# Performance work log

Measured on AMD Instinct MI355X. Metric: run time of the kernel, lower is better.

The kernel has to match this reference:

```python
import jax, jax.numpy as jnp
import numpy as np

# Sampled-neighborhood cascade sizes (src->dst per layer) and edge counts
N0, N1, N2, N3 = 400000, 200000, 100000, 50000
E1, E2, E3 = 500000, 300000, 150000
DIN, DH = 128, 128


def setup_inputs() -> dict:
    key = jax.random.key(0)
    ks = jax.random.split(key, 24)
    inp = {}
    inp['x'] = jax.random.normal(ks[0], (N0, DIN), jnp.float32)
    inp['src1'] = jax.random.randint(ks[1], (E1,), 0, N0, dtype=jnp.int64)
    inp['dst1'] = jax.random.randint(ks[2], (E1,), 0, N1, dtype=jnp.int64)
    inp['src2'] = jax.random.randint(ks[3], (E2,), 0, N1, dtype=jnp.int64)
    inp['dst2'] = jax.random.randint(ks[4], (E2,), 0, N2, dtype=jnp.int64)
    inp['src3'] = jax.random.randint(ks[5], (E3,), 0, N2, dtype=jnp.int64)
    inp['dst3'] = jax.random.randint(ks[6], (E3,), 0, N3, dtype=jnp.int64)
    # SAGEConv params: lin_l (on aggregated neighbors, with bias), lin_r (root, no bias)
    dims = [(DIN, DH), (DH, DH), (DH, DH)]
    for i, (di, do) in enumerate(dims, start=1):
        s = 1.0 / np.sqrt(di)
        inp[f'Wl{i}'] = jax.random.uniform(ks[6 + 4 * i - 3], (di, do), jnp.float32, -s, s)
        inp[f'Wr{i}'] = jax.random.uniform(ks[6 + 4 * i - 2], (di, do), jnp.float32, -s, s)
        inp[f'b{i}'] = jax.random.uniform(ks[6 + 4 * i - 1], (do,), jnp.float32, -s, s)
        inp[f'a{i}'] = jnp.full((do,), 0.25, jnp.float32)  # PReLU per-channel init
    return inp


def _sage_prelu(x_src, n_dst, src, dst, Wl, Wr, b, alpha):
    # mean aggregation over incoming edges (PyG SAGEConv default aggr='mean')
    x_dst = x_src[:n_dst]                                   # [n_dst, d]
    msg = x_src[src]                                        # [E, d] gather
    summed = jax.ops.segment_sum(msg, dst, num_segments=n_dst)
    cnt = jax.ops.segment_sum(jnp.ones(src.shape[0], x_src.dtype), dst,
                              num_segments=n_dst)
    mean = summed / jnp.maximum(cnt, 1.0)[:, None]
    out = mean @ Wl + b + x_dst @ Wr                        # lin_l(aggr) + lin_r(root)
    return jnp.where(out > 0, out, alpha * out)             # per-channel PReLU


def reference(x, src1, dst1, src2, dst2, src3, dst3,
              Wl1, Wr1, b1, a1, Wl2, Wr2, b2, a2, Wl3, Wr3, b3, a3):
    h = _sage_prelu(x, N1, src1, dst1, Wl1, Wr1, b1, a1)
    h = _sage_prelu(h, N2, src2, dst2, Wl2, Wr2, b2, a2)
    h = _sage_prelu(h, N3, src3, dst3, Wl3, Wr3, b3, a3)
    return h  # [N3, DH]
```

## Files before the change

### kernel.cpp

```cpp
#include <hip/hip_runtime.h>


constexpr int cN0 = 400000, cN1 = 200000, cN2 = 100000, cN3 = 50000;
constexpr int cE1 = 500000, cE2 = 300000, cE3 = 150000;
constexpr int cNT = cN1 + cN2 + cN3;
constexpr int cET = cE1 + cE2 + cE3;

#define NDIV_UP(a, b) (((a) + (b) - 1) / (b))

typedef __attribute__((ext_vector_type(8))) short bf16x8;
typedef __attribute__((ext_vector_type(4))) float f32x4;
typedef __attribute__((ext_vector_type(4))) unsigned u32x4;

__device__ __forceinline__ unsigned fbits(float f) {
  return __builtin_bit_cast(unsigned, f);
}
__device__ __forceinline__ float ffrom(unsigned u) {
  return __builtin_bit_cast(float, u);
}
__device__ __forceinline__ unsigned short f2bf(float f) {
  unsigned u = fbits(f);
  unsigned r = u + 0x7FFFu + ((u >> 16) & 1u);
  return (unsigned short)(r >> 16);
}
__device__ __forceinline__ float bf2f(unsigned short h) {
  return ffrom((unsigned)h << 16);
}

__global__ void detect_idx64_kernel(const long long* __restrict__ p, int E,
                                    long long nmax, int* __restrict__ flag) {
  int t = threadIdx.x;
  int n = E < 512 ? E : 512;
  int bad = 0;
  for (int i = t; i < n; i += 64) {
    long long v = p[i];
    if (v < 0 || v >= nmax) bad = 1;
  }
  unsigned long long b = __ballot(bad);
  if (t == 0) *flag = (b == 0ull) ? 1 : 0;
}

__device__ __forceinline__ int load_idx(const void* p, int i, int flag) {
  return flag ? (int)((const long long*)p)[i] : ((const int*)p)[i];
}

__global__ void hist3_kernel(const void* __restrict__ d1, const void* __restrict__ d2,
                             const void* __restrict__ d3, const int* __restrict__ flag,
                             int* __restrict__ CNT) {
  int e = blockIdx.x * 256 + threadIdx.x;
  if (e >= cET) return;
  int f = *flag;
  int d;
  if (e < cE1) d = load_idx(d1, e, f);
  else if (e < cE1 + cE2) d = cN1 + load_idx(d2, e - cE1, f);
  else d = cN1 + cN2 + load_idx(d3, e - cE1 - cE2, f);
  atomicAdd(&CNT[d], 1);
}

__global__ __launch_bounds__(256) void scan_reduce(const int* __restrict__ cnt,
                                                   int n, int* __restrict__ bsum) {
  __shared__ int s[256];
  int t = threadIdx.x;
  int base = blockIdx.x * 1024 + t * 4;
  int v = 0;
  if (base + 3 < n) {
    int4 c = *(const int4*)(cnt + base);
    v = c.x + c.y + c.z + c.w;
  } else {
    for (int i = 0; i < 4; ++i)
      if (base + i < n) v += cnt[base + i];
  }
  s[t] = v;
  __syncthreads();
  for (int off = 128; off > 0; off >>= 1) {
    if (t < off) s[t] += s[t + off];
    __syncthreads();
  }
  if (t == 0) bsum[blockIdx.x] = s[0];
}

__global__ __launch_bounds__(256) void scan_bsums(int* __restrict__ bsum, int nb) {
  __shared__ int s[256];
  int t = threadIdx.x;
  int v0 = (2 * t < nb) ? bsum[2 * t] : 0;
  int v1 = (2 * t + 1 < nb) ? bsum[2 * t + 1] : 0;
  int p = v0 + v1;
  s[t] = p;
  __syncthreads();
  for (int off = 1; off < 256; off <<= 1) {
    int x = (t >= off) ? s[t - off] : 0;
    __syncthreads();
    s[t] += x;
    __syncthreads();
  }
  int excl = s[t] - p;
  if (2 * t < nb) bsum[2 * t] = excl;
  if (2 * t + 1 < nb) bsum[2 * t + 1] = excl + v0;
}

__global__ __launch_bounds__(256) void scan_final(const int* __restrict__ cnt,
                                                  int n, const int* __restrict__ bsum,
                                                  int* __restrict__ offs) {
  __shared__ int s[256];
  int t = threadIdx.x;
  int base = blockIdx.x * 1024 + t * 4;
  int v0 = 0, v1 = 0, v2 = 0, v3 = 0;
  if (base + 3 < n) {
    int4 c = *(const int4*)(cnt + base);
    v0 = c.x; v1 = c.y; v2 = c.z; v3 = c.w;
  } else {
    if (base + 0 < n) v0 = cnt[base + 0];
    if (base + 1 < n) v1 = cnt[base + 1];
    if (base + 2 < n) v2 = cnt[base + 2];
  }
  int tsum = v0 + v1 + v2 + v3;
  s[t] = tsum;
  __syncthreads();
  for (int off = 1; off < 256; off <<= 1) {
    int x = (t >= off) ? s[t - off] : 0;
    __syncthreads();
    s[t] += x;
    __syncthreads();
  }
  int excl = s[t] - tsum;
  int o = bsum[blockIdx.x] + excl;
  if (base + 0 < n) offs[base + 0] = o;
  o += v0;
  if (base + 1 < n) offs[base + 1] = o;
  o += v1;
  if (base + 2 < n) offs[base + 2] = o;
  o += v2;
  if (base + 3 < n) offs[base + 3] = o;
}

__global__ void fill3_kernel(const void* __restrict__ s1, const void* __restrict__ d1,
                             const void* __restrict__ s2, const void* __restrict__ d2,
                             const void* __restrict__ s3, const void* __restrict__ d3,
                             const int* __restrict__ flag,
                             int* __restrict__ OFFS, int* __restrict__ EID) {
  int e = blockIdx.x * 256 + threadIdx.x;
  if (e >= cET) return;
  int f = *flag;
  int s, d;
  if (e < cE1) {
    s = load_idx(s1, e, f);
    d = load_idx(d1, e, f);
  } else if (e < cE1 + cE2) {
    int i = e - cE1;
    s = load_idx(s2, i, f);
    d = cN1 + load_idx(d2, i, f);
  } else {
    int i = e - cE1 - cE2;
    s = load_idx(s3, i, f);
    d = cN1 + cN2 + load_idx(d3, i, f);
  }
  int pos = atomicAdd(&OFFS[d], 1);
  EID[pos] = s;
}

__global__ void pack_w3_kernel(const float* __restrict__ Wl1, const float* __restrict__ Wr1,
                               const float* __restrict__ Wl2, const float* __restrict__ Wr2,
                               const float* __restrict__ Wl3, const float* __restrict__ Wr3,
                               unsigned short* __restrict__ wpk) {
  int idx = blockIdx.x * 256 + threadIdx.x;
  if (idx >= 3 * 16384) return;
  int L = idx >> 14;
  int r = idx & 16383;
  const float* Wl = L == 0 ? Wl1 : (L == 1 ? Wl2 : Wl3);
  const float* Wr = L == 0 ? Wr1 : (L == 1 ? Wr2 : Wr3);
  unsigned short* o = wpk + L * 32768;
  int j = r & 7, l = (r >> 3) & 63, cf = (r >> 9) & 7, ks = r >> 12;
  int k = ks * 32 + (l >> 4) * 8 + j;
  int col = cf * 16 + (l & 15);
  o[r] = f2bf(Wl[k * 128 + col]);
  o[16384 + r] = f2bf(Wr[k * 128 + col]);
}

__global__ __launch_bounds__(256) void fused_kernel(
    const float* __restrict__ hsrc, const int* __restrict__ OFFS,
    const int* __restrict__ EID, int rowoff,
    const unsigned short* __restrict__ W,
    const float* __restrict__ bias, const float* __restrict__ alpha,
    float* __restrict__ out, int n) {
  const int lane = threadIdx.x & 63;
  const int wv = threadIdx.x >> 6;
  const int rbase = blockIdx.x * 128 + wv * 32;
  const int g = lane >> 4;
  const int r16 = lane & 15;

  bf16x8 mh[2][4], ml[2][4];
#pragma unroll
  for (int t = 0; t < 2; ++t) {
    const int row = rbase + t * 16 + r16;
    float s[4][8];
#pragma unroll
    for (int ks = 0; ks < 4; ++ks)
#pragma unroll
      for (int j = 0; j < 8; ++j) s[ks][j] = 0.f;
    int start = 0, end = 0;
    if (row < n) {
      int gr = rowoff + row;
      start = gr ? OFFS[gr - 1] : 0;
      end = OFFS[gr];
    }
    for (int i = start; i < end; ++i) {
      const float* rp = hsrc + (size_t)EID[i] * 128 + g * 8;
#pragma unroll
      for (int ks = 0; ks < 4; ++ks) {
        const float4 v0 = *(const float4*)(rp + ks * 32);
        const float4 v1 = *(const float4*)(rp + ks * 32 + 4);
        s[ks][0] += v0.x; s[ks][1] += v0.y; s[ks][2] += v0.z; s[ks][3] += v0.w;
        s[ks][4] += v1.x; s[ks][5] += v1.y; s[ks][6] += v1.z; s[ks][7] += v1.w;
      }
    }
    const float inv = (end > start) ? 1.0f / (float)(end - start) : 0.0f;
#pragma unroll
    for (int ks = 0; ks < 4; ++ks) {
      u32x4 hwv, lwv;
#pragma unroll
      for (int p = 0; p < 4; ++p) {
        float me = s[ks][2 * p] * inv, mo = s[ks][2 * p + 1] * inv;
        unsigned ue = fbits(me), uo = fbits(mo);
        hwv[p] = (ue >> 16) | (uo & 0xFFFF0000u);
        float re = me - ffrom(ue & 0xFFFF0000u);
        float ro = mo - ffrom(uo & 0xFFFF0000u);
        lwv[p] = (fbits(re) >> 16) | (fbits(ro) & 0xFFFF0000u);
      }
      mh[t][ks] = __builtin_bit_cast(bf16x8, hwv);
      ml[t][ks] = __builtin_bit_cast(bf16x8, lwv);
    }
  }

  f32x4 acc[2][8] = {};
  for (int ks = 0; ks < 4; ++ks) {
    bf16x8 xh[2], xl[2];
#pragma unroll
    for (int t = 0; t < 2; ++t) {
      const int row = rbase + t * 16 + r16;
      if (row < n) {
        const float* xp = hsrc + (size_t)row * 128 + ks * 32 + g * 8;
        float xv[8];
        *(float4*)&xv[0] = *(const float4*)(xp);
        *(float4*)&xv[4] = *(const float4*)(xp + 4);
        u32x4 hwv, lwv;
#pragma unroll
        for (int p = 0; p < 4; ++p) {
          unsigned ue = fbits(xv[2 * p]), uo = fbits(xv[2 * p + 1]);
          hwv[p] = (ue >> 16) | (uo & 0xFFFF0000u);
          float re = xv[2 * p] - ffrom(ue & 0xFFFF0000u);
          float ro = xv[2 * p + 1] - ffrom(uo & 0xFFFF0000u);
          lwv[p] = (fbits(re) >> 16) | (fbits(ro) & 0xFFFF0000u);
        }
        xh[t] = __builtin_bit_cast(bf16x8, hwv);
        xl[t] = __builtin_bit_cast(bf16x8, lwv);
      } else {
        xh[t] = (bf16x8)0;
        xl[t] = (bf16x8)0;
      }
    }
    const unsigned short* wb = W + (size_t)ks * 4096 + (size_t)lane * 8;
#pragma unroll
    for (int cf = 0; cf < 8; ++cf) {
      const unsigned short* wp = wb + cf * 512;
      bf16x8 wl = *(const bf16x8*)(wp);
      bf16x8 wr = *(const bf16x8*)(wp + 16384);
#pragma unroll
      for (int t = 0; t < 2; ++t) {
        acc[t][cf] = __builtin_amdgcn_mfma_f32_16x16x32_bf16(mh[t][ks], wl, acc[t][cf], 0, 0, 0);
        acc[t][cf] = __builtin_amdgcn_mfma_f32_16x16x32_bf16(ml[t][ks], wl, acc[t][cf], 0, 0, 0);
        acc[t][cf] = __builtin_amdgcn_mfma_f32_16x16x32_bf16(xh[t], wr, acc[t][cf], 0, 0, 0);
        acc[t][cf] = __builtin_amdgcn_mfma_f32_16x16x32_bf16(xl[t], wr, acc[t][cf], 0, 0, 0);
      }
    }
  }

  const int ocol0 = lane & 15;
  const int orow_off = (lane >> 4) * 4;
#pragma unroll
  for (int cf = 0; cf < 8; ++cf) {
    const int ocol = cf * 16 + ocol0;
    const float b = bias[ocol];
    const float a = alpha[ocol];
#pragma unroll
    for (int t = 0; t < 2; ++t) {
      const int orb = rbase + t * 16 + orow_off;
#pragma unroll
      for (int i = 0; i < 4; ++i) {
        const int orow = orb + i;
        if (orow < n) {
          float v = acc[t][cf][i] + b;
          out[(size_t)orow * 128 + ocol] = v > 0.f ? v : a * v;
        }
      }
    }
  }
}

extern "C" void kernel_launch(void* const* d_in, const int* in_sizes, int n_in,
                              void* d_out, int out_size, void* d_ws, size_t ws_size,
                              hipStream_t stream) {
  const float* x = (const float*)d_in[0];
  const void* src1 = d_in[1];
  const void* dst1 = d_in[2];
  const void* src2 = d_in[3];
  const void* dst2 = d_in[4];
  const void* src3 = d_in[5];
  const void* dst3 = d_in[6];
  const float* Wl1 = (const float*)d_in[7];
  const float* Wr1 = (const float*)d_in[8];
  const float* b1  = (const float*)d_in[9];
  const float* a1  = (const float*)d_in[10];
  const float* Wl2 = (const float*)d_in[11];
  const float* Wr2 = (const float*)d_in[12];
  const float* b2  = (const float*)d_in[13];
  const float* a2  = (const float*)d_in[14];
  const float* Wl3 = (const float*)d_in[15];
  const float* Wr3 = (const float*)d_in[16];
  const float* b3  = (const float*)d_in[17];
  const float* a3  = (const float*)d_in[18];

  float* R1 = (float*)d_ws;
  float* R2 = R1 + (size_t)cN1 * 128;
  int* CNT = (int*)(R2 + (size_t)cN2 * 128);
  int* OFFS = CNT + cNT;
  int* EID = OFFS + cNT;
  int* bsum = EID + cET;
  int* flag = bsum + 1024;
  unsigned short* wpk = (unsigned short*)(flag + 64);

  const int nb = NDIV_UP(cNT, 1024);

  detect_idx64_kernel<<<1, 64, 0, stream>>>((const long long*)src1, cE1,
                                            (long long)cN0, flag);
  pack_w3_kernel<<<192, 256, 0, stream>>>(Wl1, Wr1, Wl2, Wr2, Wl3, Wr3, wpk);
  hipMemsetAsync(CNT, 0, (size_t)cNT * sizeof(int), stream);
  hist3_kernel<<<NDIV_UP(cET, 256), 256, 0, stream>>>(dst1, dst2, dst3, flag, CNT);
  scan_reduce<<<nb, 256, 0, stream>>>(CNT, cNT, bsum);
  scan_bsums<<<1, 256, 0, stream>>>(bsum, nb);
  scan_final<<<nb, 256, 0, stream>>>(CNT, cNT, bsum, OFFS);
  fill3_kernel<<<NDIV_UP(cET, 256), 256, 0, stream>>>(src1, dst1, src2, dst2,
                                                      src3, dst3, flag, OFFS, EID);

  fused_kernel<<<NDIV_UP(cN1, 128), 256, 0, stream>>>(
      x, OFFS, EID, 0, wpk, b1, a1, R1, cN1);
  fused_kernel<<<NDIV_UP(cN2, 128), 256, 0, stream>>>(
      R1, OFFS, EID, cN1, wpk + 32768, b2, a2, R2, cN2);
  fused_kernel<<<NDIV_UP(cN3, 128), 256, 0, stream>>>(
      R2, OFFS, EID, cN1 + cN2, wpk + 65536, b3, a3, (float*)d_out, cN3);
}
```

Before: 410.1 us.

## Split gather from GEMM, store bf16 intermediates, drop hi/lo split MFMA

```diff
diff --git a/kernel.cpp b/kernel.cpp
--- a/kernel.cpp
+++ b/kernel.cpp
@@ -22,9 +22,6 @@
   unsigned u = fbits(f);
   unsigned r = u + 0x7FFFu + ((u >> 16) & 1u);
   return (unsigned short)(r >> 16);
-}
-__device__ __forceinline__ float bf2f(unsigned short h) {
-  return ffrom((unsigned)h << 16);
 }
 
 __global__ void detect_idx64_kernel(const long long* __restrict__ p, int E,
@@ -176,86 +173,87 @@
   o[16384 + r] = f2bf(Wr[k * 128 + col]);
 }
 
-__global__ __launch_bounds__(256) void fused_kernel(
-    const float* __restrict__ hsrc, const int* __restrict__ OFFS,
+template <bool SRCF32>
+__global__ __launch_bounds__(256) void gather_kernel(
+    const void* __restrict__ hsrc, const int* __restrict__ OFFS,
     const int* __restrict__ EID, int rowoff,
+    unsigned short* __restrict__ meanB, int n) {
+  int row = blockIdx.x * 4 + (threadIdx.x >> 6);
+  if (row >= n) return;
+  int lane = threadIdx.x & 63;
+  int gr = rowoff + row;
+  int start = gr ? OFFS[gr - 1] : 0;
+  int end = OFFS[gr];
+  float a0 = 0.f, a1 = 0.f, b0 = 0.f, b1 = 0.f;
+  int i = start;
+  for (; i + 1 < end; i += 2) {
+    int s0 = EID[i], s1 = EID[i + 1];
+    if (SRCF32) {
+      float2 v0 = *(const float2*)((const float*)hsrc + (size_t)s0 * 128 + lane * 2);
+      float2 v1 = *(const float2*)((const float*)hsrc + (size_t)s1 * 128 + lane * 2);
+      a0 += v0.x; a1 += v0.y;
+      b0 += v1.x; b1 += v1.y;
+    } else {
+      unsigned u0 = *(const unsigned*)((const unsigned short*)hsrc + (size_t)s0 * 128 + lane * 2);
+      unsigned u1 = *(const unsigned*)((const unsigned short*)hsrc + (size_t)s1 * 128 + lane * 2);
+      a0 += ffrom(u0 << 16); a1 += ffrom(u0 & 0xFFFF0000u);
+      b0 += ffrom(u1 << 16); b1 += ffrom(u1 & 0xFFFF0000u);
+    }
+  }
+  if (i < end) {
+    int s0 = EID[i];
+    if (SRCF32) {
+      float2 v0 = *(const float2*)((const float*)hsrc + (size_t)s0 * 128 + lane * 2);
+      a0 += v0.x; a1 += v0.y;
+    } else {
+      unsigned u0 = *(const unsigned*)((const unsigned short*)hsrc + (size_t)s0 * 128 + lane * 2);
+      a0 += ffrom(u0 << 16); a1 += ffrom(u0 & 0xFFFF0000u);
+    }
+  }
+  a0 += b0; a1 += b1;
+  float inv = (end > start) ? 1.0f / (float)(end - start) : 0.0f;
+  unsigned o = (unsigned)f2bf(a0 * inv) | ((unsigned)f2bf(a1 * inv) << 16);
+  *(unsigned*)(meanB + (size_t)row * 128 + lane * 2) = o;
+}
+
+template <bool XF32, bool OUTF32>
+__global__ __launch_bounds__(256) void gemm_kernel(
+    const unsigned short* __restrict__ meanB, const void* __restrict__ xsrc,
     const unsigned short* __restrict__ W,
     const float* __restrict__ bias, const float* __restrict__ alpha,
-    float* __restrict__ out, int n) {
+    void* __restrict__ outp, int n) {
   const int lane = threadIdx.x & 63;
   const int wv = threadIdx.x >> 6;
   const int rbase = blockIdx.x * 128 + wv * 32;
   const int g = lane >> 4;
   const int r16 = lane & 15;
 
-  bf16x8 mh[2][4], ml[2][4];
-#pragma unroll
-  for (int t = 0; t < 2; ++t) {
-    const int row = rbase + t * 16 + r16;
-    float s[4][8];
-#pragma unroll
-    for (int ks = 0; ks < 4; ++ks)
-#pragma unroll
-      for (int j = 0; j < 8; ++j) s[ks][j] = 0.f;
-    int start = 0, end = 0;
-    if (row < n) {
-      int gr = rowoff + row;
-      start = gr ? OFFS[gr - 1] : 0;
-      end = OFFS[gr];
-    }
-    for (int i = start; i < end; ++i) {
-      const float* rp = hsrc + (size_t)EID[i] * 128 + g * 8;
-#pragma unroll
-      for (int ks = 0; ks < 4; ++ks) {
-        const float4 v0 = *(const float4*)(rp + ks * 32);
-        const float4 v1 = *(const float4*)(rp + ks * 32 + 4);
-        s[ks][0] += v0.x; s[ks][1] += v0.y; s[ks][2] += v0.z; s[ks][3] += v0.w;
-        s[ks][4] += v1.x; s[ks][5] += v1.y; s[ks][6] += v1.z; s[ks][7] += v1.w;
-      }
-    }
-    const float inv = (end > start) ? 1.0f / (float)(end - start) : 0.0f;
-#pragma unroll
-    for (int ks = 0; ks < 4; ++ks) {
-      u32x4 hwv, lwv;
-#pragma unroll
-      for (int p = 0; p < 4; ++p) {
-        float me = s[ks][2 * p] * inv, mo = s[ks][2 * p + 1] * inv;
-        unsigned ue = fbits(me), uo = fbits(mo);
-        hwv[p] = (ue >> 16) | (uo & 0xFFFF0000u);
-        float re = me - ffrom(ue & 0xFFFF0000u);
-        float ro = mo - ffrom(uo & 0xFFFF0000u);
-        lwv[p] = (fbits(re) >> 16) | (fbits(ro) & 0xFFFF0000u);
-      }
-      mh[t][ks] = __builtin_bit_cast(bf16x8, hwv);
-      ml[t][ks] = __builtin_bit_cast(bf16x8, lwv);
-    }
-  }
-
   f32x4 acc[2][8] = {};
+
   for (int ks = 0; ks < 4; ++ks) {
-    bf16x8 xh[2], xl[2];
+    bf16x8 am[2], ax[2];
 #pragma unroll
     for (int t = 0; t < 2; ++t) {
       const int row = rbase + t * 16 + r16;
       if (row < n) {
-        const float* xp = hsrc + (size_t)row * 128 + ks * 32 + g * 8;
-        float xv[8];
-        *(float4*)&xv[0] = *(const float4*)(xp);
-        *(float4*)&xv[4] = *(const float4*)(xp + 4);
-        u32x4 hwv, lwv;
-#pragma unroll
-        for (int p = 0; p < 4; ++p) {
-          unsigned ue = fbits(xv[2 * p]), uo = fbits(xv[2 * p + 1]);
-          hwv[p] = (ue >> 16) | (uo & 0xFFFF0000u);
-          float re = xv[2 * p] - ffrom(ue & 0xFFFF0000u);
-          float ro = xv[2 * p + 1] - ffrom(uo & 0xFFFF0000u);
-          lwv[p] = (fbits(re) >> 16) | (fbits(ro) & 0xFFFF0000u);
+        am[t] = *(const bf16x8*)(meanB + (size_t)row * 128 + ks * 32 + g * 8);
+        if (XF32) {
+          const float* xp = (const float*)xsrc + (size_t)row * 128 + ks * 32 + g * 8;
+          float xv[8];
+          *(float4*)&xv[0] = *(const float4*)(xp);
+          *(float4*)&xv[4] = *(const float4*)(xp + 4);
+          u32x4 w;
+#pragma unroll
+          for (int p = 0; p < 4; ++p) {
+            w[p] = (unsigned)f2bf(xv[2 * p]) | ((unsigned)f2bf(xv[2 * p + 1]) << 16);
+          }
+          ax[t] = __builtin_bit_cast(bf16x8, w);
+        } else {
+          ax[t] = *(const bf16x8*)((const unsigned short*)xsrc + (size_t)row * 128 + ks * 32 + g * 8);
         }
-        xh[t] = __builtin_bit_cast(bf16x8, hwv);
-        xl[t] = __builtin_bit_cast(bf16x8, lwv);
       } else {
-        xh[t] = (bf16x8)0;
-        xl[t] = (bf16x8)0;
+        am[t] = (bf16x8)0;
+        ax[t] = (bf16x8)0;
       }
     }
     const unsigned short* wb = W + (size_t)ks * 4096 + (size_t)lane * 8;
@@ -266,10 +264,8 @@
       bf16x8 wr = *(const bf16x8*)(wp + 16384);
 #pragma unroll
       for (int t = 0; t < 2; ++t) {
-        acc[t][cf] = __builtin_amdgcn_mfma_f32_16x16x32_bf16(mh[t][ks], wl, acc[t][cf], 0, 0, 0);
-        acc[t][cf] = __builtin_amdgcn_mfma_f32_16x16x32_bf16(ml[t][ks], wl, acc[t][cf], 0, 0, 0);
-        acc[t][cf] = __builtin_amdgcn_mfma_f32_16x16x32_bf16(xh[t], wr, acc[t][cf], 0, 0, 0);
-        acc[t][cf] = __builtin_amdgcn_mfma_f32_16x16x32_bf16(xl[t], wr, acc[t][cf], 0, 0, 0);
+        acc[t][cf] = __builtin_amdgcn_mfma_f32_16x16x32_bf16(am[t], wl, acc[t][cf], 0, 0, 0);
+        acc[t][cf] = __builtin_amdgcn_mfma_f32_16x16x32_bf16(ax[t], wr, acc[t][cf], 0, 0, 0);
       }
     }
   }
@@ -289,7 +285,12 @@
         const int orow = orb + i;
         if (orow < n) {
           float v = acc[t][cf][i] + b;
-          out[(size_t)orow * 128 + ocol] = v > 0.f ? v : a * v;
+          v = v > 0.f ? v : a * v;
+          if (OUTF32) {
+            ((float*)outp)[(size_t)orow * 128 + ocol] = v;
+          } else {
+            ((unsigned short*)outp)[(size_t)orow * 128 + ocol] = f2bf(v);
+          }
         }
       }
     }
@@ -319,9 +320,10 @@
   const float* b3  = (const float*)d_in[17];
   const float* a3  = (const float*)d_in[18];
 
-  float* R1 = (float*)d_ws;
-  float* R2 = R1 + (size_t)cN1 * 128;
-  int* CNT = (int*)(R2 + (size_t)cN2 * 128);
+  unsigned short* M1 = (unsigned short*)d_ws;
+  unsigned short* M2 = M1 + (size_t)cN1 * 128;
+  unsigned short* M3 = M2 + (size_t)cN2 * 128;
+  int* CNT = (int*)(M3 + (size_t)cN3 * 128);
   int* OFFS = CNT + cNT;
   int* EID = OFFS + cNT;
   int* bsum = EID + cET;
@@ -341,10 +343,18 @@
   fill3_kernel<<<NDIV_UP(cET, 256), 256, 0, stream>>>(src1, dst1, src2, dst2,
                                                       src3, dst3, flag, OFFS, EID);
 
-  fused_kernel<<<NDIV_UP(cN1, 128), 256, 0, stream>>>(
-      x, OFFS, EID, 0, wpk, b1, a1, R1, cN1);
-  fused_kernel<<<NDIV_UP(cN2, 128), 256, 0, stream>>>(
-      R1, OFFS, EID, cN1, wpk + 32768, b2, a2, R2, cN2);
-  fused_kernel<<<NDIV_UP(cN3, 128), 256, 0, stream>>>(
-      R2, OFFS, EID, cN1 + cN2, wpk + 65536, b3, a3, (float*)d_out, cN3);
-}
+  gather_kernel<true><<<NDIV_UP(cN1, 4), 256, 0, stream>>>(
+      x, OFFS, EID, 0, M1, cN1);
+  gemm_kernel<true, false><<<NDIV_UP(cN1, 128), 256, 0, stream>>>(
+      M1, x, wpk, b1, a1, M1, cN1);
+
+  gather_kernel<false><<<NDIV_UP(cN2, 4), 256, 0, stream>>>(
+      M1, OFFS, EID, cN1, M2, cN2);
+  gemm_kernel<false, false><<<NDIV_UP(cN2, 128), 256, 0, stream>>>(
+      M2, M1, wpk + 32768, b2, a2, M2, cN2);
+
+  gather_kernel<false><<<NDIV_UP(cN3, 4), 256, 0, stream>>>(
+      M2, OFFS, EID, cN1 + cN2, M3, cN3);
+  gemm_kernel<false, true><<<NDIV_UP(cN3, 128), 256, 0, stream>>>(
+      M3, M2, wpk + 65536, b3, a3, d_out, cN3);
+}
```

New measurement: 397.5 us. 1.03x faster.
